# Kernel optimization log

Hardware: AMD Instinct MI355X
Metric: run time of the kernel (lower is better)

The kernel has to match this reference:

```python
import jax, jax.numpy as jnp
import numpy as np

N = 50000
E = 1600000
IN_DIM = 128
HID = 64


def setup_inputs() -> dict:
    key = jax.random.key(0)
    ks = jax.random.split(key, 8)
    x = jax.random.normal(ks[0], (N, IN_DIM), dtype=jnp.float32)
    edge_row = jax.random.randint(ks[1], (E,), 0, N, dtype=jnp.int32)
    edge_col = jax.random.randint(ks[2], (E,), 0, N, dtype=jnp.int32)
    edge_val = jax.random.uniform(ks[3], (E,), dtype=jnp.float32)
    W1 = jax.random.normal(ks[4], (IN_DIM, HID), dtype=jnp.float32) * (1.0 / np.sqrt(IN_DIM))
    b1 = jnp.zeros((HID,), dtype=jnp.float32)
    W2 = jax.random.normal(ks[5], (HID, 1), dtype=jnp.float32) * (1.0 / np.sqrt(HID))
    b2 = jnp.zeros((1,), dtype=jnp.float32)
    return {"x": x, "edge_row": edge_row, "edge_col": edge_col,
            "edge_val": edge_val, "W1": W1, "b1": b1, "W2": W2, "b2": b2}


def reference(x, edge_row, edge_col, edge_val, W1, b1, W2, b2):
    # h = tanh(x @ W1 + b1)  -> [N, HID]
    h = jnp.tanh(x @ W1 + b1)
    # sparse adjacency matmul: out[i] = sum_{e: row[e]==i} val[e] * h[col[e]]
    gathered = edge_val[:, None] * h[edge_col]            # [E, HID]
    agg = jax.ops.segment_sum(gathered, edge_row, num_segments=N)  # [N, HID]
    # final linear projection to scalar per node
    return agg @ W2 + b2                                   # [N, 1]
```

## Files before the change

### kernel.cpp

```cpp
#include <hip/hip_runtime.h>

#define IN_DIM 128
#define HID 64
#define SHIFT 7
#define RPB 128
#define NBPAD 512
#define CAP 6144
#define SBLK 256
#define NSEG 4

__global__ __launch_bounds__(256) void node_kernel(
    const float* __restrict__ x, const float* __restrict__ W1,
    const float* __restrict__ b1, const float* __restrict__ W2,
    float* __restrict__ g, int n, int* __restrict__ gcnt)
{
    __shared__ float sx[64][IN_DIM];
    __shared__ float sw[IN_DIM][HID];
    if (blockIdx.x == 0)
        for (int i = threadIdx.x; i < NBPAD; i += 256) gcnt[i] = 0;

    const int node0 = blockIdx.x * 64;

    {
        const float4* src = reinterpret_cast<const float4*>(W1);
        float4* dst = reinterpret_cast<float4*>(&sw[0][0]);
        for (int i = threadIdx.x; i < (IN_DIM * HID) / 4; i += 256) dst[i] = src[i];
    }
    for (int i = threadIdx.x; i < (64 * IN_DIM) / 4; i += 256) {
        int f  = i * 4;
        int nd = f >> 7;
        int k  = f & (IN_DIM - 1);
        int gn = min(node0 + nd, n - 1);
        *reinterpret_cast<float4*>(&sx[nd][k]) =
            *reinterpret_cast<const float4*>(x + (size_t)gn * IN_DIM + k);
    }
    __syncthreads();

    const int tx = threadIdx.x & 15;
    const int ty = threadIdx.x >> 4;

    float acc[4][4];
    #pragma unroll
    for (int j = 0; j < 4; ++j) {
        float bj = b1[tx * 4 + j];
        #pragma unroll
        for (int i = 0; i < 4; ++i) acc[i][j] = bj;
    }

    #pragma unroll 2
    for (int k = 0; k < IN_DIM; k += 4) {
        float4 xa[4], wb[4];
        #pragma unroll
        for (int i = 0; i < 4; ++i)
            xa[i] = *reinterpret_cast<const float4*>(&sx[ty * 4 + i][k]);
        #pragma unroll
        for (int j = 0; j < 4; ++j)
            wb[j] = *reinterpret_cast<const float4*>(&sw[k + j][tx * 4]);
        #pragma unroll
        for (int i = 0; i < 4; ++i) {
            acc[i][0] += xa[i].x * wb[0].x; acc[i][1] += xa[i].x * wb[0].y;
            acc[i][2] += xa[i].x * wb[0].z; acc[i][3] += xa[i].x * wb[0].w;
            acc[i][0] += xa[i].y * wb[1].x; acc[i][1] += xa[i].y * wb[1].y;
            acc[i][2] += xa[i].y * wb[1].z; acc[i][3] += xa[i].y * wb[1].w;
            acc[i][0] += xa[i].z * wb[2].x; acc[i][1] += xa[i].z * wb[2].y;
            acc[i][2] += xa[i].z * wb[2].z; acc[i][3] += xa[i].z * wb[2].w;
            acc[i][0] += xa[i].w * wb[3].x; acc[i][1] += xa[i].w * wb[3].y;
            acc[i][2] += xa[i].w * wb[3].z; acc[i][3] += xa[i].w * wb[3].w;
        }
    }

    float w2v[4];
    #pragma unroll
    for (int j = 0; j < 4; ++j) w2v[j] = W2[tx * 4 + j];
    #pragma unroll
    for (int i = 0; i < 4; ++i) {
        float s = 0.f;
        #pragma unroll
        for (int j = 0; j < 4; ++j) {
            float a = fminf(fmaxf(acc[i][j], -15.f), 15.f);
            float ex = __expf(2.f * a);
            s += ((ex - 1.f) / (ex + 1.f)) * w2v[j];
        }
        #pragma unroll
        for (int off = 1; off < 16; off <<= 1) s += __shfl_xor(s, off);
        if (tx == 0) {
            int nd = node0 + ty * 4 + i;
            if (nd < n) g[nd] = s;
        }
    }
}

__global__ __launch_bounds__(1024) void scatter_kernel(
    const int* __restrict__ erow, const int* __restrict__ ecol,
    const float* __restrict__ ev, int e, int chunk,
    int* __restrict__ gcnt, uint2* __restrict__ pairs)
{
    __shared__ int h[NBPAD];
    __shared__ int cur[NBPAD];
    for (int i = threadIdx.x; i < NBPAD; i += 1024) h[i] = 0;
    __syncthreads();
    const int s = blockIdx.x * chunk, t = min(e, s + chunk);
    const int cnt = t - s, cnt4 = cnt >> 2;

    const int4*   r4 = reinterpret_cast<const int4*>(erow + s);
    const int4*   c4 = reinterpret_cast<const int4*>(ecol + s);
    const float4* v4 = reinterpret_cast<const float4*>(ev + s);

    for (int i = threadIdx.x; i < cnt4; i += 1024) {
        int4 r = r4[i];
        atomicAdd(&h[r.x >> SHIFT], 1);
        atomicAdd(&h[r.y >> SHIFT], 1);
        atomicAdd(&h[r.z >> SHIFT], 1);
        atomicAdd(&h[r.w >> SHIFT], 1);
    }
    for (int i = s + (cnt4 << 2) + threadIdx.x; i < t; i += 1024)
        atomicAdd(&h[erow[i] >> SHIFT], 1);
    __syncthreads();
    for (int b = threadIdx.x; b < NBPAD; b += 1024)
        cur[b] = h[b] ? atomicAdd(&gcnt[b], h[b]) : 0;
    __syncthreads();

    for (int i = threadIdx.x; i < cnt4; i += 1024) {
        int4 r = r4[i]; int4 c = c4[i]; float4 v = v4[i];
        {
            int b = r.x >> SHIFT; int pos = atomicAdd(&cur[b], 1);
            if (pos < CAP) pairs[(size_t)b * CAP + pos] =
                make_uint2(((unsigned)(r.x & (RPB-1)) << 16) | (unsigned)c.x, __float_as_uint(v.x));
        }
        {
            int b = r.y >> SHIFT; int pos = atomicAdd(&cur[b], 1);
            if (pos < CAP) pairs[(size_t)b * CAP + pos] =
                make_uint2(((unsigned)(r.y & (RPB-1)) << 16) | (unsigned)c.y, __float_as_uint(v.y));
        }
        {
            int b = r.z >> SHIFT; int pos = atomicAdd(&cur[b], 1);
            if (pos < CAP) pairs[(size_t)b * CAP + pos] =
                make_uint2(((unsigned)(r.z & (RPB-1)) << 16) | (unsigned)c.z, __float_as_uint(v.z));
        }
        {
            int b = r.w >> SHIFT; int pos = atomicAdd(&cur[b], 1);
            if (pos < CAP) pairs[(size_t)b * CAP + pos] =
                make_uint2(((unsigned)(r.w & (RPB-1)) << 16) | (unsigned)c.w, __float_as_uint(v.w));
        }
    }
    for (int i = s + (cnt4 << 2) + threadIdx.x; i < t; i += 1024) {
        int r = erow[i];
        int b = r >> SHIFT; int pos = atomicAdd(&cur[b], 1);
        if (pos < CAP) pairs[(size_t)b * CAP + pos] =
            make_uint2(((unsigned)(r & (RPB-1)) << 16) | (unsigned)ecol[i], __float_as_uint(ev[i]));
    }
}

__global__ __launch_bounds__(256) void reduce_kernel(
    const uint2* __restrict__ pairs, const int* __restrict__ gcnt,
    const float* __restrict__ g, float* __restrict__ partial)
{
    __shared__ float acc[RPB];
    const int b   = blockIdx.x >> 2;
    const int seg = blockIdx.x & (NSEG - 1);
    for (int i = threadIdx.x; i < RPB; i += 256) acc[i] = 0.f;
    __syncthreads();
    const int m  = min(gcnt[b], CAP);
    const int s0 = (m * seg)       >> 2;
    const int s1 = (m * (seg + 1)) >> 2;
    const uint2* p = pairs + (size_t)b * CAP;

    int i = s0 + (int)threadIdx.x;
    for (; i + 768 < s1; i += 1024) {
        uint2 e0 = p[i], e1 = p[i + 256], e2 = p[i + 512], e3 = p[i + 768];
        float g0 = g[e0.x & 0xFFFF], g1 = g[e1.x & 0xFFFF];
        float g2 = g[e2.x & 0xFFFF], g3 = g[e3.x & 0xFFFF];
        atomicAdd(&acc[e0.x >> 16], __uint_as_float(e0.y) * g0);
        atomicAdd(&acc[e1.x >> 16], __uint_as_float(e1.y) * g1);
        atomicAdd(&acc[e2.x >> 16], __uint_as_float(e2.y) * g2);
        atomicAdd(&acc[e3.x >> 16], __uint_as_float(e3.y) * g3);
    }
    for (; i < s1; i += 256) {
        uint2 eu = p[i];
        atomicAdd(&acc[eu.x >> 16], __uint_as_float(eu.y) * g[eu.x & 0xFFFF]);
    }
    __syncthreads();
    float* pp = partial + (size_t)blockIdx.x * RPB;
    for (int k = threadIdx.x; k < RPB; k += 256) pp[k] = acc[k];
}

__global__ __launch_bounds__(256) void combine_kernel(
    const float* __restrict__ partial, const float* __restrict__ b2,
    float* __restrict__ out, int n)
{
    const int r = blockIdx.x * 256 + threadIdx.x;
    if (r >= n) return;
    const int b = r >> SHIFT, rl = r & (RPB - 1);
    const float* pp = partial + ((size_t)b * NSEG) * RPB + rl;
    out[r] = pp[0] + pp[RPB] + pp[2 * RPB] + pp[3 * RPB] + b2[0];
}

extern "C" void kernel_launch(void* const* d_in, const int* in_sizes, int n_in,
                              void* d_out, int out_size, void* d_ws, size_t ws_size,
                              hipStream_t stream) {
    const float* x    = (const float*)d_in[0];
    const int*   erow = (const int*)  d_in[1];
    const int*   ecol = (const int*)  d_in[2];
    const float* ev   = (const float*)d_in[3];
    const float* W1   = (const float*)d_in[4];
    const float* b1   = (const float*)d_in[5];
    const float* W2   = (const float*)d_in[6];
    const float* b2   = (const float*)d_in[7];
    float* out = (float*)d_out;

    const int n  = in_sizes[0] / IN_DIM;
    const int e  = in_sizes[1];
    const int nb = (n + RPB - 1) >> SHIFT;

    char* ws = (char*)d_ws;
    float* g = (float*)ws;
    size_t off = ((size_t)n * 4 + 255) & ~(size_t)255;
    int* gcnt = (int*)(ws + off); off += NBPAD * 4;
    float* partial = (float*)(ws + off); off += (size_t)NBPAD * NSEG * RPB * 4;
    uint2* pairs = (uint2*)(ws + off);

    const int chunk = (((e + SBLK - 1) / SBLK) + 3) & ~3;

    node_kernel   <<<(n + 63) / 64, 256, 0, stream>>>(x, W1, b1, W2, g, n, gcnt);
    scatter_kernel<<<SBLK, 1024, 0, stream>>>(erow, ecol, ev, e, chunk, gcnt, pairs);
    reduce_kernel <<<nb * NSEG, 256, 0, stream>>>(pairs, gcnt, g, partial);
    combine_kernel<<<(n + 255) / 256, 256, 0, stream>>>(partial, b2, out, n);
}
```

Measured before the change: 137.9 us.

## Use bf16 MFMA for node GEMM and fuse combine into reduce kernel

Converts x and W1 to bf16 in shared memory (W1 stored transposed with padding) and computes the 64-node tile with 16x16x32 bf16 MFMA instructions instead of scalar FP32 FMAs. The reduce kernel now uses one 1024-thread block per row bucket and writes the final output with the bias added, which removes the partial buffer and the separate combine launch. The aim is less node-kernel compute time and one fewer launch, at the cost of bf16 rounding in the first GEMM and fewer, larger reduce blocks (391 instead of 1564).

Result: faster. 131.1 us (-5.0%).

```diff
diff --git a/kernel.cpp b/kernel.cpp
--- a/kernel.cpp
+++ b/kernel.cpp
@@ -1,4 +1,5 @@
 #include <hip/hip_runtime.h>
+#include <hip/hip_bf16.h>
 
 #define IN_DIM 128
 #define HID 64
@@ -7,85 +8,91 @@
 #define NBPAD 512
 #define CAP 6144
 #define SBLK 256
-#define NSEG 4
+#define LDK 136
+
+typedef __attribute__((ext_vector_type(8))) short bf16x8;
+typedef __attribute__((ext_vector_type(4))) float f32x4;
+
+__device__ __forceinline__ unsigned short f2bf(float f) {
+    __hip_bfloat16 h = __float2bfloat16(f);
+    return *reinterpret_cast<unsigned short*>(&h);
+}
 
 __global__ __launch_bounds__(256) void node_kernel(
     const float* __restrict__ x, const float* __restrict__ W1,
     const float* __restrict__ b1, const float* __restrict__ W2,
     float* __restrict__ g, int n, int* __restrict__ gcnt)
 {
-    __shared__ float sx[64][IN_DIM];
-    __shared__ float sw[IN_DIM][HID];
+    __shared__ unsigned short sx[64 * LDK];
+    __shared__ unsigned short sw[HID * LDK];
     if (blockIdx.x == 0)
         for (int i = threadIdx.x; i < NBPAD; i += 256) gcnt[i] = 0;
 
     const int node0 = blockIdx.x * 64;
 
-    {
-        const float4* src = reinterpret_cast<const float4*>(W1);
-        float4* dst = reinterpret_cast<float4*>(&sw[0][0]);
-        for (int i = threadIdx.x; i < (IN_DIM * HID) / 4; i += 256) dst[i] = src[i];
-    }
-    for (int i = threadIdx.x; i < (64 * IN_DIM) / 4; i += 256) {
-        int f  = i * 4;
-        int nd = f >> 7;
-        int k  = f & (IN_DIM - 1);
-        int gn = min(node0 + nd, n - 1);
-        *reinterpret_cast<float4*>(&sx[nd][k]) =
-            *reinterpret_cast<const float4*>(x + (size_t)gn * IN_DIM + k);
-    }
-    __syncthreads();
-
-    const int tx = threadIdx.x & 15;
-    const int ty = threadIdx.x >> 4;
-
-    float acc[4][4];
-    #pragma unroll
-    for (int j = 0; j < 4; ++j) {
-        float bj = b1[tx * 4 + j];
-        #pragma unroll
-        for (int i = 0; i < 4; ++i) acc[i][j] = bj;
-    }
-
-    #pragma unroll 2
-    for (int k = 0; k < IN_DIM; k += 4) {
-        float4 xa[4], wb[4];
-        #pragma unroll
-        for (int i = 0; i < 4; ++i)
-            xa[i] = *reinterpret_cast<const float4*>(&sx[ty * 4 + i][k]);
-        #pragma unroll
-        for (int j = 0; j < 4; ++j)
-            wb[j] = *reinterpret_cast<const float4*>(&sw[k + j][tx * 4]);
-        #pragma unroll
-        for (int i = 0; i < 4; ++i) {
-            acc[i][0] += xa[i].x * wb[0].x; acc[i][1] += xa[i].x * wb[0].y;
-            acc[i][2] += xa[i].x * wb[0].z; acc[i][3] += xa[i].x * wb[0].w;
-            acc[i][0] += xa[i].y * wb[1].x; acc[i][1] += xa[i].y * wb[1].y;
-            acc[i][2] += xa[i].y * wb[1].z; acc[i][3] += xa[i].y * wb[1].w;
-            acc[i][0] += xa[i].z * wb[2].x; acc[i][1] += xa[i].z * wb[2].y;
-            acc[i][2] += xa[i].z * wb[2].z; acc[i][3] += xa[i].z * wb[2].w;
-            acc[i][0] += xa[i].w * wb[3].x; acc[i][1] += xa[i].w * wb[3].y;
-            acc[i][2] += xa[i].w * wb[3].z; acc[i][3] += xa[i].w * wb[3].w;
-        }
-    }
-
-    float w2v[4];
-    #pragma unroll
-    for (int j = 0; j < 4; ++j) w2v[j] = W2[tx * 4 + j];
-    #pragma unroll
-    for (int i = 0; i < 4; ++i) {
-        float s = 0.f;
-        #pragma unroll
-        for (int j = 0; j < 4; ++j) {
-            float a = fminf(fmaxf(acc[i][j], -15.f), 15.f);
+    for (int i = threadIdx.x; i < 64 * 16; i += 256) {
+        int r = i >> 4, c = i & 15;
+        int gn = min(node0 + r, n - 1);
+        const float4* src = reinterpret_cast<const float4*>(x + (size_t)gn * IN_DIM + c * 8);
+        float4 f0 = src[0], f1 = src[1];
+        union { unsigned short u[8]; uint4 v; } pk;
+        pk.u[0] = f2bf(f0.x); pk.u[1] = f2bf(f0.y);
+        pk.u[2] = f2bf(f0.z); pk.u[3] = f2bf(f0.w);
+        pk.u[4] = f2bf(f1.x); pk.u[5] = f2bf(f1.y);
+        pk.u[6] = f2bf(f1.z); pk.u[7] = f2bf(f1.w);
+        *reinterpret_cast<uint4*>(&sx[r * LDK + c * 8]) = pk.v;
+    }
+    for (int i = threadIdx.x; i < IN_DIM * HID; i += 256) {
+        int k = i >> 6, h = i & 63;
+        sw[h * LDK + k] = f2bf(W1[i]);
+    }
+
+    const int wv = threadIdx.x >> 6;
+    const int ln = threadIdx.x & 63;
+    const int lg = ln >> 4;
+    const int li = ln & 15;
+    const int rowl = wv * 16 + li;
+    const int kb0 = lg * 8;
+
+    f32x4 acc[4];
+    #pragma unroll
+    for (int t = 0; t < 4; ++t) {
+        float bj = b1[t * 16 + li];
+        acc[t] = (f32x4){bj, bj, bj, bj};
+    }
+    __syncthreads();
+
+    #pragma unroll
+    for (int ks = 0; ks < 4; ++ks) {
+        bf16x8 af = *reinterpret_cast<const bf16x8*>(&sx[rowl * LDK + ks * 32 + kb0]);
+        #pragma unroll
+        for (int t = 0; t < 4; ++t) {
+            bf16x8 bfv = *reinterpret_cast<const bf16x8*>(&sw[(t * 16 + li) * LDK + ks * 32 + kb0]);
+            acc[t] = __builtin_amdgcn_mfma_f32_16x16x32_bf16(af, bfv, acc[t], 0, 0, 0);
+        }
+    }
+
+    float s[4] = {0.f, 0.f, 0.f, 0.f};
+    #pragma unroll
+    for (int t = 0; t < 4; ++t) {
+        float w2 = W2[t * 16 + li];
+        #pragma unroll
+        for (int r = 0; r < 4; ++r) {
+            float a = fminf(fmaxf(acc[t][r], -15.f), 15.f);
             float ex = __expf(2.f * a);
-            s += ((ex - 1.f) / (ex + 1.f)) * w2v[j];
-        }
-        #pragma unroll
-        for (int off = 1; off < 16; off <<= 1) s += __shfl_xor(s, off);
-        if (tx == 0) {
-            int nd = node0 + ty * 4 + i;
-            if (nd < n) g[nd] = s;
+            s[r] += ((ex - 1.f) / (ex + 1.f)) * w2;
+        }
+    }
+    #pragma unroll
+    for (int off = 1; off < 16; off <<= 1) {
+        #pragma unroll
+        for (int r = 0; r < 4; ++r) s[r] += __shfl_xor(s[r], off);
+    }
+    if (li == 0) {
+        #pragma unroll
+        for (int r = 0; r < 4; ++r) {
+            int nd = node0 + wv * 16 + lg * 4 + r;
+            if (nd < n) g[nd] = s[r];
         }
     }
 }
@@ -151,23 +158,21 @@
     }
 }
 
-__global__ __launch_bounds__(256) void reduce_kernel(
+__global__ __launch_bounds__(1024) void reduce_kernel(
     const uint2* __restrict__ pairs, const int* __restrict__ gcnt,
-    const float* __restrict__ g, float* __restrict__ partial)
+    const float* __restrict__ g, const float* __restrict__ b2,
+    float* __restrict__ out, int n)
 {
     __shared__ float acc[RPB];
-    const int b   = blockIdx.x >> 2;
-    const int seg = blockIdx.x & (NSEG - 1);
-    for (int i = threadIdx.x; i < RPB; i += 256) acc[i] = 0.f;
-    __syncthreads();
-    const int m  = min(gcnt[b], CAP);
-    const int s0 = (m * seg)       >> 2;
-    const int s1 = (m * (seg + 1)) >> 2;
+    const int b = blockIdx.x;
+    if (threadIdx.x < RPB) acc[threadIdx.x] = 0.f;
+    __syncthreads();
+    const int m = min(gcnt[b], CAP);
     const uint2* p = pairs + (size_t)b * CAP;
 
-    int i = s0 + (int)threadIdx.x;
-    for (; i + 768 < s1; i += 1024) {
-        uint2 e0 = p[i], e1 = p[i + 256], e2 = p[i + 512], e3 = p[i + 768];
+    int i = threadIdx.x;
+    for (; i + 3072 < m; i += 4096) {
+        uint2 e0 = p[i], e1 = p[i + 1024], e2 = p[i + 2048], e3 = p[i + 3072];
         float g0 = g[e0.x & 0xFFFF], g1 = g[e1.x & 0xFFFF];
         float g2 = g[e2.x & 0xFFFF], g3 = g[e3.x & 0xFFFF];
         atomicAdd(&acc[e0.x >> 16], __uint_as_float(e0.y) * g0);
@@ -175,24 +180,15 @@
         atomicAdd(&acc[e2.x >> 16], __uint_as_float(e2.y) * g2);
         atomicAdd(&acc[e3.x >> 16], __uint_as_float(e3.y) * g3);
     }
-    for (; i < s1; i += 256) {
+    for (; i < m; i += 1024) {
         uint2 eu = p[i];
         atomicAdd(&acc[eu.x >> 16], __uint_as_float(eu.y) * g[eu.x & 0xFFFF]);
     }
     __syncthreads();
-    float* pp = partial + (size_t)blockIdx.x * RPB;
-    for (int k = threadIdx.x; k < RPB; k += 256) pp[k] = acc[k];
-}
-
-__global__ __launch_bounds__(256) void combine_kernel(
-    const float* __restrict__ partial, const float* __restrict__ b2,
-    float* __restrict__ out, int n)
-{
-    const int r = blockIdx.x * 256 + threadIdx.x;
-    if (r >= n) return;
-    const int b = r >> SHIFT, rl = r & (RPB - 1);
-    const float* pp = partial + ((size_t)b * NSEG) * RPB + rl;
-    out[r] = pp[0] + pp[RPB] + pp[2 * RPB] + pp[3 * RPB] + b2[0];
+    if (threadIdx.x < RPB) {
+        int r = (b << SHIFT) + threadIdx.x;
+        if (r < n) out[r] = acc[threadIdx.x] + b2[0];
+    }
 }
 
 extern "C" void kernel_launch(void* const* d_in, const int* in_sizes, int n_in,
@@ -216,13 +212,11 @@
     float* g = (float*)ws;
     size_t off = ((size_t)n * 4 + 255) & ~(size_t)255;
     int* gcnt = (int*)(ws + off); off += NBPAD * 4;
-    float* partial = (float*)(ws + off); off += (size_t)NBPAD * NSEG * RPB * 4;
     uint2* pairs = (uint2*)(ws + off);
 
     const int chunk = (((e + SBLK - 1) / SBLK) + 3) & ~3;
 
     node_kernel   <<<(n + 63) / 64, 256, 0, stream>>>(x, W1, b1, W2, g, n, gcnt);
     scatter_kernel<<<SBLK, 1024, 0, stream>>>(erow, ecol, ev, e, chunk, gcnt, pairs);
-    reduce_kernel <<<nb * NSEG, 256, 0, stream>>>(pairs, gcnt, g, partial);
-    combine_kernel<<<(n + 255) / 256, 256, 0, stream>>>(partial, b2, out, n);
-}
+    reduce_kernel <<<nb, 1024, 0, stream>>>(pairs, gcnt, g, b2, out, n);
+}
```
